# Kernel tuning notes

Measured on AMD Instinct MI355X. Metric: run time of the kernel, lower is better.

Reference implementation:

```python
import jax, jax.numpy as jnp
import numpy as np

N, E, T, D, V, G = 100000, 400000, 4, 300, 3000, 128
EPS = 1e-5


def _lin_init(k, fin, fout):
    s = 1.0 / np.sqrt(fin)
    kw, kb = jax.random.split(k)
    w = jax.random.uniform(kw, (fin, fout), jnp.float32, -s, s)
    b = jax.random.uniform(kb, (fout,), jnp.float32, -s, s)
    return w, b


def setup_inputs() -> dict:
    key = jax.random.key(0)
    ks = jax.random.split(key, 12)
    emb = jax.random.normal(ks[0], (V, D), jnp.float32) * 0.02
    emb = emb.at[0].set(0.0)  # padding_idx=0
    ew1, eb1 = _lin_init(ks[1], 3 * D, D)
    ew2, eb2 = _lin_init(ks[2], D, D)
    n1w1, n1b1 = _lin_init(ks[3], 2 * D, D)
    n1w2, n1b2 = _lin_init(ks[4], D, D)
    n2w1, n2b1 = _lin_init(ks[5], 2 * D, D)
    n2w2, n2b2 = _lin_init(ks[6], D, D)
    ln_w = jnp.ones((D,), jnp.float32)
    ln_b = jnp.zeros((D,), jnp.float32)
    x_tok = jax.random.randint(ks[7], (N, T), 0, V)
    edge_attr_tok = jax.random.randint(ks[8], (E, T), 0, V)
    edge_index = jax.random.randint(ks[9], (2, E), 0, N)
    added_sym_edge = jax.random.randint(ks[10], (E // 2,), 0, E)
    batch = jnp.sort(jax.random.randint(ks[11], (N,), 0, G))
    return dict(x_tok=x_tok, edge_attr_tok=edge_attr_tok, edge_index=edge_index,
                added_sym_edge=added_sym_edge, batch=batch, emb=emb,
                ew1=ew1, eb1=eb1, ew2=ew2, eb2=eb2,
                n1w1=n1w1, n1b1=n1b1, n1w2=n1w2, n1b2=n1b2,
                n2w1=n2w1, n2b1=n2b1, n2w2=n2w2, n2b2=n2b2,
                ln_w=ln_w, ln_b=ln_b)


def _mlp(h, w1, b1, w2, b2):
    return jnp.maximum(h @ w1 + b1, 0.0) @ w2 + b2


def reference(x_tok, edge_attr_tok, edge_index, added_sym_edge, batch, emb,
              ew1, eb1, ew2, eb2, n1w1, n1b1, n1w2, n1b2,
              n2w1, n2b1, n2w2, n2b2, ln_w, ln_b):
    # embedding-sum over token axis
    x = emb[x_tok].sum(axis=-2)                      # [N, D]
    sign = jnp.ones((E,), emb.dtype).at[added_sym_edge].set(-1.0)
    ea = (emb[edge_attr_tok] * sign[:, None, None]).sum(axis=-2)  # [E, D]

    row, col = edge_index[0], edge_index[1]
    # EdgeModel: cat([src, dest, edge_attr]) -> MLP
    e_in = jnp.concatenate([x[row], x[col], ea], axis=1)  # [E, 3D]
    edge_enc = _mlp(e_in, ew1, eb1, ew2, eb2)             # [E, D]

    # NodeModel: gather + MLP + scatter_mean + MLP
    m = _mlp(jnp.concatenate([x[row], edge_enc], axis=1), n1w1, n1b1, n1w2, n1b2)
    cnt = jax.ops.segment_sum(jnp.ones((E,), m.dtype), col, num_segments=N)
    agg = jax.ops.segment_sum(m, col, num_segments=N) / jnp.maximum(cnt, 1.0)[:, None]
    x_enc = _mlp(jnp.concatenate([x, agg], axis=1), n2w1, n2b1, n2w2, n2b2)  # [N, D]

    # GraphLayerNorm: normalize over all elements of each graph
    ncnt = jax.ops.segment_sum(jnp.ones((N,), x_enc.dtype), batch, num_segments=G)
    denom = jnp.maximum(ncnt * D, 1.0)
    mean = jax.ops.segment_sum(x_enc.sum(axis=-1), batch, num_segments=G) / denom
    xc = x_enc - mean[batch][:, None]
    var = jax.ops.segment_sum((xc * xc).sum(axis=-1), batch, num_segments=G) / denom
    x_out = xc / jnp.sqrt(var + EPS)[batch][:, None] * ln_w + ln_b
    return x_out, edge_enc
```

## Files before the change

kernel.cpp:

```cpp
#include <hip/hip_runtime.h>


constexpr int N_NODES = 100000;
constexpr int N_EDGES = 400000;
constexpr int TOKS    = 4;
constexpr int D       = 300;
constexpr int NG      = 128;
constexpr float EPSV  = 1e-5f;

typedef __attribute__((ext_vector_type(8))) short bh8;
typedef __attribute__((ext_vector_type(4))) float fx4;

constexpr size_t AGG_OFF  = 0;
constexpr size_t CNT_OFF  = AGG_OFF + (size_t)N_NODES * D;
constexpr size_t GSUM_OFF = CNT_OFF + N_NODES;
constexpr size_t GSQ_OFF  = GSUM_OFF + NG;
constexpr size_t GCNT_OFF = GSQ_OFF + NG;
constexpr size_t SIGN_OFF = GCNT_OFF + NG;
constexpr size_t X_OFF    = SIGN_OFF + N_EDGES;
constexpr size_t PACK_OFF = X_OFF + (size_t)N_NODES * D;
constexpr size_t ZERO_FLOATS = SIGN_OFF;

constexpr size_t P_SEC3 = 30ull * 20 * 64 * 8;
constexpr size_t P_SEC2 = 20ull * 20 * 64 * 8;
constexpr size_t P_SEC1 = 10ull * 20 * 64 * 8;

__device__ inline unsigned short f2bf(float f) {
    unsigned int u = __float_as_uint(f);
    return (unsigned short)((u + 0x7fffu + ((u >> 16) & 1u)) >> 16);
}
__device__ inline float bf2f(unsigned short s) {
    return __uint_as_float(((unsigned int)s) << 16);
}

__global__ void fill_sign_k(float* sign) {
    int i = blockIdx.x * blockDim.x + threadIdx.x;
    if (i < N_EDGES) sign[i] = 1.0f;
}

__global__ void scatter_sign_k(const int* __restrict__ ase, float* sign) {
    int i = blockIdx.x * blockDim.x + threadIdx.x;
    if (i < N_EDGES / 2) sign[ase[i]] = -1.0f;
}

__global__ void embsum_k(const int* __restrict__ tok, const float* __restrict__ emb,
                         const float* __restrict__ sign, float* out, int nrows) {
    int idx = blockIdx.x * blockDim.x + threadIdx.x;
    int total = nrows * D;
    if (idx >= total) return;
    int r = idx / D;
    int d = idx - r * D;
    const int* t = tok + r * TOKS;
    float s = emb[(size_t)t[0] * D + d] + emb[(size_t)t[1] * D + d]
            + emb[(size_t)t[2] * D + d] + emb[(size_t)t[3] * D + d];
    if (sign) s *= sign[r];
    out[idx] = s;
}

__global__ void count_col_k(const int* __restrict__ coli, float* cnt) {
    int i = blockIdx.x * blockDim.x + threadIdx.x;
    if (i < N_EDGES) atomicAdd(&cnt[coli[i]], 1.0f);
}

__global__ void pack_w_k(const float* __restrict__ W, unsigned short* __restrict__ out,
                         int secs) {
    int idx = blockIdx.x * blockDim.x + threadIdx.x;
    int total = secs * 12800;
    if (idx >= total) return;
    int lane = idx & 63;
    int nt = (idx >> 6) % 20;
    int kt = idx / 1280;
    int col = nt * 16 + (lane & 15);
    int kg = (lane >> 4) * 8;
#pragma unroll
    for (int j = 0; j < 8; ++j) {
        int p = kt * 32 + kg + j;
        int sec = p / 320;
        int kk = p - sec * 320;
        float w = 0.f;
        if (kk < 300 && col < 300) w = W[(size_t)(sec * 300 + kk) * 300 + col];
        out[(size_t)idx * 8 + j] = f2bf(w);
    }
}

template <int SECS, int MODE, bool SCATTER>
__global__ __launch_bounds__(256, 2) void mlp_mfma_k(
        const float* __restrict__ x, const float* aux,
        const int* __restrict__ rowi, const int* __restrict__ coli,
        const float* __restrict__ cnt,
        const unsigned short* __restrict__ W1p, const float* __restrict__ b1,
        const unsigned short* __restrict__ W2p, const float* __restrict__ b2,
        float* outp, int nrows)
{
    constexpr int NCHUNK = SECS * 5;
    __shared__ __align__(16) unsigned short Ahi[4096];
    __shared__ __align__(16) unsigned short Alo[4096];
    __shared__ __align__(16) unsigned short Hs[64 * 328];
    __shared__ int Ridx[64];
    __shared__ int Cidx[64];
    __shared__ float Icnt[64];

    const int tid  = threadIdx.x;
    const int wave = tid >> 6;
    const int lane = tid & 63;
    const int r0   = blockIdx.x * 64;

    if (tid < 64) {
        int e = r0 + tid; if (e >= nrows) e = nrows - 1;
        if constexpr (MODE == 0 || MODE == 1) { Ridx[tid] = rowi[e]; Cidx[tid] = coli[e]; }
        else { Icnt[tid] = 1.0f / fmaxf(cnt[e], 1.0f); }
    }
    for (int i = tid; i < 64 * 20; i += 256)
        Hs[(i / 20) * 328 + 300 + (i % 20)] = 0;
    __syncthreads();

    const int sm  = tid >> 2;
    const int sko = (tid & 3) << 4;
    const int skt   = sko >> 5;
    const int sg0   = (sko & 31) >> 3;
    const int smt   = sm >> 4;
    const int sbase = ((skt * 4 + smt) * 64 + (sm & 15) + sg0 * 16) * 8;
    int se = r0 + sm; if (se >= nrows) se = nrows - 1;

    fx4 acc[4][5];
#pragma unroll
    for (int a = 0; a < 4; ++a)
#pragma unroll
        for (int b = 0; b < 5; ++b) acc[a][b] = fx4{0.f, 0.f, 0.f, 0.f};

    for (int c = 0; c < NCHUNK; ++c) {
        {
            int sec = (c * 64) / 320;
            int kk0 = c * 64 - sec * 320 + sko;
            const float* base;
            if constexpr (MODE == 0) {
                base = (sec == 0) ? x + (size_t)Ridx[sm] * 300
                     : (sec == 1) ? x + (size_t)Cidx[sm] * 300
                                  : aux + (size_t)se * 300;
            } else if constexpr (MODE == 1) {
                base = (sec == 0) ? x + (size_t)Ridx[sm] * 300
                                  : aux + (size_t)se * 300;
            } else {
                base = (sec == 0) ? x + (size_t)se * 300 : aux + (size_t)se * 300;
            }
            float f[16];
            if (kk0 + 16 <= 300) {
                const float4* p = (const float4*)(base + kk0);
                float4 q0 = p[0], q1 = p[1], q2 = p[2], q3 = p[3];
                f[0]=q0.x; f[1]=q0.y; f[2]=q0.z; f[3]=q0.w;
                f[4]=q1.x; f[5]=q1.y; f[6]=q1.z; f[7]=q1.w;
                f[8]=q2.x; f[9]=q2.y; f[10]=q2.z; f[11]=q2.w;
                f[12]=q3.x; f[13]=q3.y; f[14]=q3.z; f[15]=q3.w;
            } else {
#pragma unroll
                for (int i = 0; i < 16; ++i) {
                    int kk = kk0 + i;
                    f[i] = (kk < 300) ? base[kk] : 0.f;
                }
            }
            if constexpr (MODE == 2) {
                float scale = (sec == 1) ? Icnt[sm] : 1.0f;
#pragma unroll
                for (int i = 0; i < 16; ++i) f[i] *= scale;
            }
            bh8 vh0, vl0, vh1, vl1;
#pragma unroll
            for (int i = 0; i < 8; ++i) {
                unsigned short h0 = f2bf(f[i]);
                vh0[i] = (short)h0;
                vl0[i] = (short)f2bf(f[i] - bf2f(h0));
                unsigned short h1 = f2bf(f[8 + i]);
                vh1[i] = (short)h1;
                vl1[i] = (short)f2bf(f[8 + i] - bf2f(h1));
            }
            *(bh8*)&Ahi[sbase]       = vh0;
            *(bh8*)&Ahi[sbase + 128] = vh1;
            *(bh8*)&Alo[sbase]       = vl0;
            *(bh8*)&Alo[sbase + 128] = vl1;
        }
        __syncthreads();
#pragma unroll
        for (int kt = 0; kt < 2; ++kt) {
            const int ktg = c * 2 + kt;
            bh8 bfr[5];
#pragma unroll
            for (int nt = 0; nt < 5; ++nt)
                bfr[nt] = *(const bh8*)(W1p + (((size_t)ktg * 20 + wave * 5 + nt) * 64 + lane) * 8);
#pragma unroll
            for (int mt = 0; mt < 4; ++mt) {
                bh8 ah = *(const bh8*)&Ahi[((kt * 4 + mt) * 64 + lane) * 8];
                bh8 al = *(const bh8*)&Alo[((kt * 4 + mt) * 64 + lane) * 8];
#pragma unroll
                for (int nt = 0; nt < 5; ++nt) {
                    acc[mt][nt] = __builtin_amdgcn_mfma_f32_16x16x32_bf16(ah, bfr[nt], acc[mt][nt], 0, 0, 0);
                    acc[mt][nt] = __builtin_amdgcn_mfma_f32_16x16x32_bf16(al, bfr[nt], acc[mt][nt], 0, 0, 0);
                }
            }
        }
        __syncthreads();
    }

    {
        const int rg = (lane >> 4) * 4;
#pragma unroll
        for (int nt = 0; nt < 5; ++nt) {
            int col = (wave * 5 + nt) * 16 + (lane & 15);
            if (col < 300) {
                float bb = b1[col];
#pragma unroll
                for (int mt = 0; mt < 4; ++mt)
#pragma unroll
                    for (int r = 0; r < 4; ++r) {
                        float v = fmaxf(acc[mt][nt][r] + bb, 0.f);
                        Hs[(mt * 16 + rg + r) * 328 + col] = f2bf(v);
                    }
            }
        }
    }
    __syncthreads();

    fx4 acc2[4][5];
#pragma unroll
    for (int a = 0; a < 4; ++a)
#pragma unroll
        for (int b = 0; b < 5; ++b) acc2[a][b] = fx4{0.f, 0.f, 0.f, 0.f};

    for (int kt = 0; kt < 10; ++kt) {
        bh8 bfr[5];
#pragma unroll
        for (int nt = 0; nt < 5; ++nt)
            bfr[nt] = *(const bh8*)(W2p + (((size_t)kt * 20 + wave * 5 + nt) * 64 + lane) * 8);
#pragma unroll
        for (int mt = 0; mt < 4; ++mt) {
            bh8 ah = *(const bh8*)&Hs[(mt * 16 + (lane & 15)) * 328 + kt * 32 + (lane >> 4) * 8];
#pragma unroll
            for (int nt = 0; nt < 5; ++nt)
                acc2[mt][nt] = __builtin_amdgcn_mfma_f32_16x16x32_bf16(ah, bfr[nt], acc2[mt][nt], 0, 0, 0);
        }
    }

    {
        const int rg = (lane >> 4) * 4;
#pragma unroll
        for (int nt = 0; nt < 5; ++nt) {
            int col = (wave * 5 + nt) * 16 + (lane & 15);
            if (col >= 300) continue;
            float bb = b2[col];
#pragma unroll
            for (int mt = 0; mt < 4; ++mt)
#pragma unroll
                for (int r = 0; r < 4; ++r) {
                    int m = mt * 16 + rg + r;
                    int e = r0 + m;
                    if (e >= nrows) continue;
                    float v = acc2[mt][nt][r] + bb;
                    if constexpr (SCATTER) atomicAdd(&outp[(size_t)Cidx[m] * 300 + col], v);
                    else                   outp[(size_t)e * 300 + col] = v;
                }
        }
    }
}

__global__ __launch_bounds__(256) void graph_stats_k(
        const float* __restrict__ xe, const int* __restrict__ batch,
        float* gsum, float* gsq, float* gcnt) {
    int n = blockIdx.x;
    int tid = threadIdx.x;
    float v = 0.f, v2 = 0.f;
    for (int d = tid; d < D; d += 256) {
        float t = xe[(size_t)n * D + d];
        v += t; v2 += t * t;
    }
    for (int off = 32; off > 0; off >>= 1) {
        v  += __shfl_down(v, off, 64);
        v2 += __shfl_down(v2, off, 64);
    }
    __shared__ float s1[4], s2[4];
    int w = tid >> 6, l = tid & 63;
    if (l == 0) { s1[w] = v; s2[w] = v2; }
    __syncthreads();
    if (tid == 0) {
        float a = s1[0] + s1[1] + s1[2] + s1[3];
        float b = s2[0] + s2[1] + s2[2] + s2[3];
        int g = batch[n];
        atomicAdd(&gsum[g], a);
        atomicAdd(&gsq[g], b);
        atomicAdd(&gcnt[g], 1.0f);
    }
}

__global__ void graph_norm_k(float* xe, const int* __restrict__ batch,
                             const float* __restrict__ gsum, const float* __restrict__ gsq,
                             const float* __restrict__ gcnt,
                             const float* __restrict__ lnw, const float* __restrict__ lnb) {
    int idx = blockIdx.x * blockDim.x + threadIdx.x;
    if (idx >= N_NODES * D) return;
    int n = idx / D;
    int d = idx - n * D;
    int g = batch[n];
    float denom = fmaxf(gcnt[g] * (float)D, 1.0f);
    float mean = gsum[g] / denom;
    float var  = gsq[g] / denom - mean * mean;
    float r = rsqrtf(var + EPSV);
    xe[idx] = (xe[idx] - mean) * r * lnw[d] + lnb[d];
}

extern "C" void kernel_launch(void* const* d_in, const int* in_sizes, int n_in,
                              void* d_out, int out_size, void* d_ws, size_t ws_size,
                              hipStream_t stream) {
    const int*   x_tok  = (const int*)d_in[0];
    const int*   ea_tok = (const int*)d_in[1];
    const int*   eidx   = (const int*)d_in[2];
    const int*   ase    = (const int*)d_in[3];
    const int*   batch  = (const int*)d_in[4];
    const float* emb    = (const float*)d_in[5];
    const float* ew1  = (const float*)d_in[6];
    const float* eb1  = (const float*)d_in[7];
    const float* ew2  = (const float*)d_in[8];
    const float* eb2  = (const float*)d_in[9];
    const float* n1w1 = (const float*)d_in[10];
    const float* n1b1 = (const float*)d_in[11];
    const float* n1w2 = (const float*)d_in[12];
    const float* n1b2 = (const float*)d_in[13];
    const float* n2w1 = (const float*)d_in[14];
    const float* n2b1 = (const float*)d_in[15];
    const float* n2w2 = (const float*)d_in[16];
    const float* n2b2 = (const float*)d_in[17];
    const float* lnw  = (const float*)d_in[18];
    const float* lnb  = (const float*)d_in[19];

    const int* rowi = eidx;
    const int* coli = eidx + N_EDGES;

    float* out  = (float*)d_out;
    float* xout = out;
    float* eenc = out + (size_t)N_NODES * D;

    float* ws   = (float*)d_ws;
    float* agg  = ws + AGG_OFF;
    float* cnt  = ws + CNT_OFF;
    float* gsum = ws + GSUM_OFF;
    float* gsq  = ws + GSQ_OFF;
    float* gcnt = ws + GCNT_OFF;
    float* sign = ws + SIGN_OFF;
    float* x    = ws + X_OFF;

    unsigned short* ew1p  = (unsigned short*)(ws + PACK_OFF);
    unsigned short* ew2p  = ew1p  + P_SEC3;
    unsigned short* n1w1p = ew2p  + P_SEC1;
    unsigned short* n1w2p = n1w1p + P_SEC2;
    unsigned short* n2w1p = n1w2p + P_SEC1;
    unsigned short* n2w2p = n2w1p + P_SEC2;

    pack_w_k<<<(3 * 12800 + 255) / 256, 256, 0, stream>>>(ew1,  ew1p,  3);
    pack_w_k<<<(1 * 12800 + 255) / 256, 256, 0, stream>>>(ew2,  ew2p,  1);
    pack_w_k<<<(2 * 12800 + 255) / 256, 256, 0, stream>>>(n1w1, n1w1p, 2);
    pack_w_k<<<(1 * 12800 + 255) / 256, 256, 0, stream>>>(n1w2, n1w2p, 1);
    pack_w_k<<<(2 * 12800 + 255) / 256, 256, 0, stream>>>(n2w1, n2w1p, 2);
    pack_w_k<<<(1 * 12800 + 255) / 256, 256, 0, stream>>>(n2w2, n2w2p, 1);

    hipMemsetAsync(ws, 0, ZERO_FLOATS * sizeof(float), stream);

    fill_sign_k<<<(N_EDGES + 255) / 256, 256, 0, stream>>>(sign);
    scatter_sign_k<<<(N_EDGES / 2 + 255) / 256, 256, 0, stream>>>(ase, sign);

    embsum_k<<<(N_NODES * D + 255) / 256, 256, 0, stream>>>(x_tok, emb, nullptr, x, N_NODES);
    embsum_k<<<(N_EDGES * D + 255) / 256, 256, 0, stream>>>(ea_tok, emb, sign, eenc, N_EDGES);

    mlp_mfma_k<3, 0, false><<<N_EDGES / 64, 256, 0, stream>>>(
        x, eenc, rowi, coli, nullptr, ew1p, eb1, ew2p, eb2, eenc, N_EDGES);

    count_col_k<<<(N_EDGES + 255) / 256, 256, 0, stream>>>(coli, cnt);

    mlp_mfma_k<2, 1, true><<<N_EDGES / 64, 256, 0, stream>>>(
        x, eenc, rowi, coli, nullptr, n1w1p, n1b1, n1w2p, n1b2, agg, N_EDGES);

    mlp_mfma_k<2, 2, false><<<(N_NODES + 63) / 64, 256, 0, stream>>>(
        x, agg, nullptr, nullptr, cnt, n2w1p, n2b1, n2w2p, n2b2, xout, N_NODES);

    graph_stats_k<<<N_NODES, 256, 0, stream>>>(xout, batch, gsum, gsq, gcnt);
    graph_norm_k<<<(N_NODES * D + 255) / 256, 256, 0, stream>>>(
        xout, batch, gsum, gsq, gcnt, lnw, lnb);
}
```

Measured before the change: 4.022 ms.

## Fuse edge embedding and graph stats into MLP kernels, double-buffer A tiles

```diff
diff --git a/kernel.cpp b/kernel.cpp
--- a/kernel.cpp
+++ b/kernel.cpp
@@ -3,7 +3,6 @@
 
 constexpr int N_NODES = 100000;
 constexpr int N_EDGES = 400000;
-constexpr int TOKS    = 4;
 constexpr int D       = 300;
 constexpr int NG      = 128;
 constexpr float EPSV  = 1e-5f;
@@ -29,9 +28,6 @@
     unsigned int u = __float_as_uint(f);
     return (unsigned short)((u + 0x7fffu + ((u >> 16) & 1u)) >> 16);
 }
-__device__ inline float bf2f(unsigned short s) {
-    return __uint_as_float(((unsigned int)s) << 16);
-}
 
 __global__ void fill_sign_k(float* sign) {
     int i = blockIdx.x * blockDim.x + threadIdx.x;
@@ -43,18 +39,22 @@
     if (i < N_EDGES / 2) sign[ase[i]] = -1.0f;
 }
 
-__global__ void embsum_k(const int* __restrict__ tok, const float* __restrict__ emb,
-                         const float* __restrict__ sign, float* out, int nrows) {
+__global__ void embsum4_k(const int* __restrict__ tok, const float* __restrict__ emb,
+                          float* out, int nrows) {
     int idx = blockIdx.x * blockDim.x + threadIdx.x;
-    int total = nrows * D;
+    int total = nrows * 75;
     if (idx >= total) return;
-    int r = idx / D;
-    int d = idx - r * D;
-    const int* t = tok + r * TOKS;
-    float s = emb[(size_t)t[0] * D + d] + emb[(size_t)t[1] * D + d]
-            + emb[(size_t)t[2] * D + d] + emb[(size_t)t[3] * D + d];
-    if (sign) s *= sign[r];
-    out[idx] = s;
+    int r = idx / 75;
+    int q = (idx - r * 75) * 4;
+    int4 t = *(const int4*)(tok + (size_t)r * 4);
+    float4 a = *(const float4*)(emb + (size_t)t.x * D + q);
+    float4 b = *(const float4*)(emb + (size_t)t.y * D + q);
+    float4 c = *(const float4*)(emb + (size_t)t.z * D + q);
+    float4 d = *(const float4*)(emb + (size_t)t.w * D + q);
+    float4 o;
+    o.x = a.x + b.x + c.x + d.x; o.y = a.y + b.y + c.y + d.y;
+    o.z = a.z + b.z + c.z + d.z; o.w = a.w + b.w + c.w + d.w;
+    *(float4*)(out + (size_t)r * D + q) = o;
 }
 
 __global__ void count_col_k(const int* __restrict__ coli, float* cnt) {
@@ -84,101 +84,139 @@
 }
 
 template <int SECS, int MODE, bool SCATTER>
-__global__ __launch_bounds__(256, 2) void mlp_mfma_k(
-        const float* __restrict__ x, const float* aux,
+__global__ __launch_bounds__(256, (MODE == 0) ? 2 : 3) void mlp_mfma_k(
+        const float* __restrict__ x, const float* __restrict__ aux,
         const int* __restrict__ rowi, const int* __restrict__ coli,
-        const float* __restrict__ cnt,
+        const float* __restrict__ cnt, const float* __restrict__ sign,
+        const int* __restrict__ eatok, const float* __restrict__ emb,
         const unsigned short* __restrict__ W1p, const float* __restrict__ b1,
         const unsigned short* __restrict__ W2p, const float* __restrict__ b2,
-        float* outp, int nrows)
+        float* outp, const int* __restrict__ batch,
+        float* gsum, float* gsq, float* gcnt, int nrows)
 {
     constexpr int NCHUNK = SECS * 5;
-    __shared__ __align__(16) unsigned short Ahi[4096];
-    __shared__ __align__(16) unsigned short Alo[4096];
-    __shared__ __align__(16) unsigned short Hs[64 * 328];
-    __shared__ int Ridx[64];
+    __shared__ __align__(16) unsigned short SM[20480];
     __shared__ int Cidx[64];
-    __shared__ float Icnt[64];
+    __shared__ float RS[64], RQ[64];
 
     const int tid  = threadIdx.x;
     const int wave = tid >> 6;
     const int lane = tid & 63;
     const int r0   = blockIdx.x * 64;
 
-    if (tid < 64) {
-        int e = r0 + tid; if (e >= nrows) e = nrows - 1;
-        if constexpr (MODE == 0 || MODE == 1) { Ridx[tid] = rowi[e]; Cidx[tid] = coli[e]; }
-        else { Icnt[tid] = 1.0f / fmaxf(cnt[e], 1.0f); }
-    }
-    for (int i = tid; i < 64 * 20; i += 256)
-        Hs[(i / 20) * 328 + 300 + (i % 20)] = 0;
-    __syncthreads();
-
     const int sm  = tid >> 2;
     const int sko = (tid & 3) << 4;
-    const int skt   = sko >> 5;
-    const int sg0   = (sko & 31) >> 3;
-    const int smt   = sm >> 4;
-    const int sbase = ((skt * 4 + smt) * 64 + (sm & 15) + sg0 * 16) * 8;
+    const int sbase = (((sko >> 5) * 4 + (sm >> 4)) * 64 + (sm & 15) + ((sko & 31) >> 3) * 16) * 8;
     int se = r0 + sm; if (se >= nrows) se = nrows - 1;
 
+    if (tid < 64) {
+        if constexpr (SCATTER) {
+            int e = r0 + tid; if (e >= nrows) e = nrows - 1;
+            Cidx[tid] = coli[e];
+        }
+        RS[tid] = 0.f; RQ[tid] = 0.f;
+    }
+
+    const float* sb0; const float* sb1;
+    const float *et0, *et1, *et2, *et3;
+    float sgn = 1.f, icnt = 1.f;
+    if constexpr (MODE == 0) {
+        sb0 = x + (size_t)rowi[se] * D;
+        sb1 = x + (size_t)coli[se] * D;
+        int4 tk = *(const int4*)(eatok + (size_t)se * 4);
+        et0 = emb + (size_t)tk.x * D; et1 = emb + (size_t)tk.y * D;
+        et2 = emb + (size_t)tk.z * D; et3 = emb + (size_t)tk.w * D;
+        sgn = sign[se];
+    } else if constexpr (MODE == 1) {
+        sb0 = x + (size_t)rowi[se] * D;
+        sb1 = aux + (size_t)se * D;
+    } else {
+        sb0 = x + (size_t)se * D;
+        sb1 = aux + (size_t)se * D;
+        icnt = 1.0f / fmaxf(cnt[se], 1.0f);
+    }
+
+    float4 G[(MODE == 0) ? 16 : 4];
+    float  f[16];
+
+    auto issuef = [&](int c) {
+        int s = c / 5;
+        int kk0 = (c - s * 5) * 64 + sko;
+        if constexpr (MODE == 0) {
+            if (s == 2) {
+#pragma unroll
+                for (int q = 0; q < 4; ++q) {
+                    int kk = kk0 + q * 4;
+                    bool ok = (kk + 4 <= 300);
+                    G[q]      = ok ? *(const float4*)(et0 + kk) : make_float4(0.f, 0.f, 0.f, 0.f);
+                    G[4 + q]  = ok ? *(const float4*)(et1 + kk) : make_float4(0.f, 0.f, 0.f, 0.f);
+                    G[8 + q]  = ok ? *(const float4*)(et2 + kk) : make_float4(0.f, 0.f, 0.f, 0.f);
+                    G[12 + q] = ok ? *(const float4*)(et3 + kk) : make_float4(0.f, 0.f, 0.f, 0.f);
+                }
+                return;
+            }
+        }
+        const float* b = (s == 0) ? sb0 : sb1;
+#pragma unroll
+        for (int q = 0; q < 4; ++q) {
+            int kk = kk0 + q * 4;
+            G[q] = (kk + 4 <= 300) ? *(const float4*)(b + kk) : make_float4(0.f, 0.f, 0.f, 0.f);
+        }
+    };
+
+    auto finishf = [&](int c) {
+        int s = c / 5;
+#pragma unroll
+        for (int q = 0; q < 4; ++q) {
+            float4 v = G[q];
+            if constexpr (MODE == 0) {
+                if (s == 2) {
+                    float4 t1 = G[4 + q], t2 = G[8 + q], t3 = G[12 + q];
+                    v.x = sgn * (v.x + t1.x + t2.x + t3.x);
+                    v.y = sgn * (v.y + t1.y + t2.y + t3.y);
+                    v.z = sgn * (v.z + t1.z + t2.z + t3.z);
+                    v.w = sgn * (v.w + t1.w + t2.w + t3.w);
+                }
+            }
+            if constexpr (MODE == 2) {
+                if (s == 1) { v.x *= icnt; v.y *= icnt; v.z *= icnt; v.w *= icnt; }
+            }
+            f[q * 4 + 0] = v.x; f[q * 4 + 1] = v.y; f[q * 4 + 2] = v.z; f[q * 4 + 3] = v.w;
+        }
+    };
+
+    auto convertf = [&](int buf) {
+        unsigned int uh[8], ul[8];
+#pragma unroll
+        for (int j = 0; j < 8; ++j) {
+            float a = f[2 * j], b = f[2 * j + 1];
+            unsigned int ua = __float_as_uint(a), ub = __float_as_uint(b);
+            uh[j] = __builtin_amdgcn_perm(ub, ua, 0x07060302u);
+            float la = a - __uint_as_float(ua & 0xffff0000u);
+            float lb = b - __uint_as_float(ub & 0xffff0000u);
+            ul[j] = __builtin_amdgcn_perm(__float_as_uint(lb), __float_as_uint(la), 0x07060302u);
+        }
+        int b0 = buf * 8192;
+        *(uint4*)&SM[b0 + sbase]              = make_uint4(uh[0], uh[1], uh[2], uh[3]);
+        *(uint4*)&SM[b0 + sbase + 128]        = make_uint4(uh[4], uh[5], uh[6], uh[7]);
+        *(uint4*)&SM[b0 + 4096 + sbase]       = make_uint4(ul[0], ul[1], ul[2], ul[3]);
+        *(uint4*)&SM[b0 + 4096 + sbase + 128] = make_uint4(ul[4], ul[5], ul[6], ul[7]);
+    };
+
     fx4 acc[4][5];
 #pragma unroll
     for (int a = 0; a < 4; ++a)
 #pragma unroll
         for (int b = 0; b < 5; ++b) acc[a][b] = fx4{0.f, 0.f, 0.f, 0.f};
 
+    issuef(0);
+    finishf(0);
+    convertf(0);
+    __syncthreads();
+
     for (int c = 0; c < NCHUNK; ++c) {
-        {
-            int sec = (c * 64) / 320;
-            int kk0 = c * 64 - sec * 320 + sko;
-            const float* base;
-            if constexpr (MODE == 0) {
-                base = (sec == 0) ? x + (size_t)Ridx[sm] * 300
-                     : (sec == 1) ? x + (size_t)Cidx[sm] * 300
-                                  : aux + (size_t)se * 300;
-            } else if constexpr (MODE == 1) {
-                base = (sec == 0) ? x + (size_t)Ridx[sm] * 300
-                                  : aux + (size_t)se * 300;
-            } else {
-                base = (sec == 0) ? x + (size_t)se * 300 : aux + (size_t)se * 300;
-            }
-            float f[16];
-            if (kk0 + 16 <= 300) {
-                const float4* p = (const float4*)(base + kk0);
-                float4 q0 = p[0], q1 = p[1], q2 = p[2], q3 = p[3];
-                f[0]=q0.x; f[1]=q0.y; f[2]=q0.z; f[3]=q0.w;
-                f[4]=q1.x; f[5]=q1.y; f[6]=q1.z; f[7]=q1.w;
-                f[8]=q2.x; f[9]=q2.y; f[10]=q2.z; f[11]=q2.w;
-                f[12]=q3.x; f[13]=q3.y; f[14]=q3.z; f[15]=q3.w;
-            } else {
-#pragma unroll
-                for (int i = 0; i < 16; ++i) {
-                    int kk = kk0 + i;
-                    f[i] = (kk < 300) ? base[kk] : 0.f;
-                }
-            }
-            if constexpr (MODE == 2) {
-                float scale = (sec == 1) ? Icnt[sm] : 1.0f;
-#pragma unroll
-                for (int i = 0; i < 16; ++i) f[i] *= scale;
-            }
-            bh8 vh0, vl0, vh1, vl1;
-#pragma unroll
-            for (int i = 0; i < 8; ++i) {
-                unsigned short h0 = f2bf(f[i]);
-                vh0[i] = (short)h0;
-                vl0[i] = (short)f2bf(f[i] - bf2f(h0));
-                unsigned short h1 = f2bf(f[8 + i]);
-                vh1[i] = (short)h1;
-                vl1[i] = (short)f2bf(f[8 + i] - bf2f(h1));
-            }
-            *(bh8*)&Ahi[sbase]       = vh0;
-            *(bh8*)&Ahi[sbase + 128] = vh1;
-            *(bh8*)&Alo[sbase]       = vl0;
-            *(bh8*)&Alo[sbase + 128] = vl1;
-        }
-        __syncthreads();
+        const int cur = c & 1;
+        if (c + 1 < NCHUNK) issuef(c + 1);
 #pragma unroll
         for (int kt = 0; kt < 2; ++kt) {
             const int ktg = c * 2 + kt;
@@ -188,8 +226,8 @@
                 bfr[nt] = *(const bh8*)(W1p + (((size_t)ktg * 20 + wave * 5 + nt) * 64 + lane) * 8);
 #pragma unroll
             for (int mt = 0; mt < 4; ++mt) {
-                bh8 ah = *(const bh8*)&Ahi[((kt * 4 + mt) * 64 + lane) * 8];
-                bh8 al = *(const bh8*)&Alo[((kt * 4 + mt) * 64 + lane) * 8];
+                bh8 ah = *(const bh8*)&SM[cur * 8192 + ((kt * 4 + mt) * 64 + lane) * 8];
+                bh8 al = *(const bh8*)&SM[cur * 8192 + 4096 + ((kt * 4 + mt) * 64 + lane) * 8];
 #pragma unroll
                 for (int nt = 0; nt < 5; ++nt) {
                     acc[mt][nt] = __builtin_amdgcn_mfma_f32_16x16x32_bf16(ah, bfr[nt], acc[mt][nt], 0, 0, 0);
@@ -197,33 +235,41 @@
                 }
             }
         }
+        if (c + 1 < NCHUNK) {
+            finishf(c + 1);
+            convertf(cur ^ 1);
+        }
         __syncthreads();
     }
 
+    const int rg = (lane >> 4) * 4;
+    for (int i = tid; i < 64 * 20; i += 256) {
+        int row = i / 20, h = 300 + (i % 20);
+        SM[((h >> 5) * 4 + ((h >> 3) & 3)) * 512 + row * 8 + (h & 7)] = 0;
+    }
     {
-        const int rg = (lane >> 4) * 4;
 #pragma unroll
         for (int nt = 0; nt < 5; ++nt) {
             int col = (wave * 5 + nt) * 16 + (lane & 15);
             if (col < 300) {
                 float bb = b1[col];
+                int hoff = ((col >> 5) * 4 + ((col >> 3) & 3)) * 512 + (col & 7);
 #pragma unroll
                 for (int mt = 0; mt < 4; ++mt)
 #pragma unroll
                     for (int r = 0; r < 4; ++r) {
                         float v = fmaxf(acc[mt][nt][r] + bb, 0.f);
-                        Hs[(mt * 16 + rg + r) * 328 + col] = f2bf(v);
+                        SM[hoff + (mt * 16 + rg + r) * 8] = f2bf(v);
                     }
             }
         }
     }
     __syncthreads();
 
-    fx4 acc2[4][5];
 #pragma unroll
     for (int a = 0; a < 4; ++a)
 #pragma unroll
-        for (int b = 0; b < 5; ++b) acc2[a][b] = fx4{0.f, 0.f, 0.f, 0.f};
+        for (int b = 0; b < 5; ++b) acc[a][b] = fx4{0.f, 0.f, 0.f, 0.f};
 
     for (int kt = 0; kt < 10; ++kt) {
         bh8 bfr[5];
@@ -232,77 +278,85 @@
             bfr[nt] = *(const bh8*)(W2p + (((size_t)kt * 20 + wave * 5 + nt) * 64 + lane) * 8);
 #pragma unroll
         for (int mt = 0; mt < 4; ++mt) {
-            bh8 ah = *(const bh8*)&Hs[(mt * 16 + (lane & 15)) * 328 + kt * 32 + (lane >> 4) * 8];
+            bh8 ah = *(const bh8*)&SM[((kt * 4 + (lane >> 4)) * 64 + mt * 16 + (lane & 15)) * 8];
 #pragma unroll
             for (int nt = 0; nt < 5; ++nt)
-                acc2[mt][nt] = __builtin_amdgcn_mfma_f32_16x16x32_bf16(ah, bfr[nt], acc2[mt][nt], 0, 0, 0);
-        }
-    }
-
-    {
-        const int rg = (lane >> 4) * 4;
-#pragma unroll
-        for (int nt = 0; nt < 5; ++nt) {
-            int col = (wave * 5 + nt) * 16 + (lane & 15);
-            if (col >= 300) continue;
-            float bb = b2[col];
-#pragma unroll
-            for (int mt = 0; mt < 4; ++mt)
-#pragma unroll
-                for (int r = 0; r < 4; ++r) {
-                    int m = mt * 16 + rg + r;
-                    int e = r0 + m;
-                    if (e >= nrows) continue;
-                    float v = acc2[mt][nt][r] + bb;
-                    if constexpr (SCATTER) atomicAdd(&outp[(size_t)Cidx[m] * 300 + col], v);
-                    else                   outp[(size_t)e * 300 + col] = v;
-                }
-        }
-    }
-}
-
-__global__ __launch_bounds__(256) void graph_stats_k(
-        const float* __restrict__ xe, const int* __restrict__ batch,
-        float* gsum, float* gsq, float* gcnt) {
-    int n = blockIdx.x;
-    int tid = threadIdx.x;
-    float v = 0.f, v2 = 0.f;
-    for (int d = tid; d < D; d += 256) {
-        float t = xe[(size_t)n * D + d];
-        v += t; v2 += t * t;
-    }
-    for (int off = 32; off > 0; off >>= 1) {
-        v  += __shfl_down(v, off, 64);
-        v2 += __shfl_down(v2, off, 64);
-    }
-    __shared__ float s1[4], s2[4];
-    int w = tid >> 6, l = tid & 63;
-    if (l == 0) { s1[w] = v; s2[w] = v2; }
-    __syncthreads();
-    if (tid == 0) {
-        float a = s1[0] + s1[1] + s1[2] + s1[3];
-        float b = s2[0] + s2[1] + s2[2] + s2[3];
-        int g = batch[n];
-        atomicAdd(&gsum[g], a);
-        atomicAdd(&gsq[g], b);
-        atomicAdd(&gcnt[g], 1.0f);
-    }
-}
-
-__global__ void graph_norm_k(float* xe, const int* __restrict__ batch,
-                             const float* __restrict__ gsum, const float* __restrict__ gsq,
-                             const float* __restrict__ gcnt,
-                             const float* __restrict__ lnw, const float* __restrict__ lnb) {
+                acc[mt][nt] = __builtin_amdgcn_mfma_f32_16x16x32_bf16(ah, bfr[nt], acc[mt][nt], 0, 0, 0);
+        }
+    }
+
+    float s1a[16], s2a[16];
+    if constexpr (MODE == 2) {
+#pragma unroll
+        for (int i = 0; i < 16; ++i) { s1a[i] = 0.f; s2a[i] = 0.f; }
+    }
+#pragma unroll
+    for (int nt = 0; nt < 5; ++nt) {
+        int col = (wave * 5 + nt) * 16 + (lane & 15);
+        if (col >= 300) continue;
+        float bb = b2[col];
+#pragma unroll
+        for (int mt = 0; mt < 4; ++mt)
+#pragma unroll
+            for (int r = 0; r < 4; ++r) {
+                int m = mt * 16 + rg + r;
+                int e = r0 + m;
+                if (e >= nrows) continue;
+                float v = acc[mt][nt][r] + bb;
+                if constexpr (SCATTER) atomicAdd(&outp[(size_t)Cidx[m] * D + col], v);
+                else                   outp[(size_t)e * D + col] = v;
+                if constexpr (MODE == 2) { s1a[mt * 4 + r] += v; s2a[mt * 4 + r] += v * v; }
+            }
+    }
+
+    if constexpr (MODE == 2) {
+#pragma unroll
+        for (int i = 0; i < 16; ++i) {
+            float s = s1a[i], q = s2a[i];
+            s += __shfl_xor(s, 1, 64); q += __shfl_xor(q, 1, 64);
+            s += __shfl_xor(s, 2, 64); q += __shfl_xor(q, 2, 64);
+            s += __shfl_xor(s, 4, 64); q += __shfl_xor(q, 4, 64);
+            s += __shfl_xor(s, 8, 64); q += __shfl_xor(q, 8, 64);
+            if ((lane & 15) == 0) {
+                int row = (i >> 2) * 16 + rg + (i & 3);
+                atomicAdd(&RS[row], s);
+                atomicAdd(&RQ[row], q);
+            }
+        }
+        __syncthreads();
+        if (tid < 64) {
+            int e = r0 + tid;
+            if (e < nrows) {
+                int g = batch[e];
+                atomicAdd(&gsum[g], RS[tid]);
+                atomicAdd(&gsq[g],  RQ[tid]);
+                atomicAdd(&gcnt[g], 1.0f);
+            }
+        }
+    }
+}
+
+__global__ void graph_norm4_k(float* xe, const int* __restrict__ batch,
+                              const float* __restrict__ gsum, const float* __restrict__ gsq,
+                              const float* __restrict__ gcnt,
+                              const float* __restrict__ lnw, const float* __restrict__ lnb) {
     int idx = blockIdx.x * blockDim.x + threadIdx.x;
-    if (idx >= N_NODES * D) return;
-    int n = idx / D;
-    int d = idx - n * D;
+    if (idx >= N_NODES * 75) return;
+    int n = idx / 75;
+    int d = (idx - n * 75) * 4;
     int g = batch[n];
     float denom = fmaxf(gcnt[g] * (float)D, 1.0f);
     float mean = gsum[g] / denom;
     float var  = gsq[g] / denom - mean * mean;
     float r = rsqrtf(var + EPSV);
-    xe[idx] = (xe[idx] - mean) * r * lnw[d] + lnb[d];
+    float4 v  = *(const float4*)(xe + (size_t)n * D + d);
+    float4 w  = *(const float4*)(lnw + d);
+    float4 bb = *(const float4*)(lnb + d);
+    v.x = (v.x - mean) * r * w.x + bb.x;
+    v.y = (v.y - mean) * r * w.y + bb.y;
+    v.z = (v.z - mean) * r * w.z + bb.z;
+    v.w = (v.w - mean) * r * w.w + bb.w;
+    *(float4*)(xe + (size_t)n * D + d) = v;
 }
 
 extern "C" void kernel_launch(void* const* d_in, const int* in_sizes, int n_in,
@@ -364,21 +418,22 @@
     fill_sign_k<<<(N_EDGES + 255) / 256, 256, 0, stream>>>(sign);
     scatter_sign_k<<<(N_EDGES / 2 + 255) / 256, 256, 0, stream>>>(ase, sign);
 
-    embsum_k<<<(N_NODES * D + 255) / 256, 256, 0, stream>>>(x_tok, emb, nullptr, x, N_NODES);
-    embsum_k<<<(N_EDGES * D + 255) / 256, 256, 0, stream>>>(ea_tok, emb, sign, eenc, N_EDGES);
+    embsum4_k<<<(N_NODES * 75 + 255) / 256, 256, 0, stream>>>(x_tok, emb, x, N_NODES);
 
     mlp_mfma_k<3, 0, false><<<N_EDGES / 64, 256, 0, stream>>>(
-        x, eenc, rowi, coli, nullptr, ew1p, eb1, ew2p, eb2, eenc, N_EDGES);
+        x, nullptr, rowi, coli, nullptr, sign, ea_tok, emb,
+        ew1p, eb1, ew2p, eb2, eenc, nullptr, nullptr, nullptr, nullptr, N_EDGES);
 
     count_col_k<<<(N_EDGES + 255) / 256, 256, 0, stream>>>(coli, cnt);
 
     mlp_mfma_k<2, 1, true><<<N_EDGES / 64, 256, 0, stream>>>(
-        x, eenc, rowi, coli, nullptr, n1w1p, n1b1, n1w2p, n1b2, agg, N_EDGES);
+        x, eenc, rowi, coli, nullptr, nullptr, nullptr, nullptr,
+        n1w1p, n1b1, n1w2p, n1b2, agg, nullptr, nullptr, nullptr, nullptr, N_EDGES);
 
     mlp_mfma_k<2, 2, false><<<(N_NODES + 63) / 64, 256, 0, stream>>>(
-        x, agg, nullptr, nullptr, cnt, n2w1p, n2b1, n2w2p, n2b2, xout, N_NODES);
-
-    graph_stats_k<<<N_NODES, 256, 0, stream>>>(xout, batch, gsum, gsq, gcnt);
-    graph_norm_k<<<(N_NODES * D + 255) / 256, 256, 0, stream>>>(
+        x, agg, nullptr, nullptr, cnt, nullptr, nullptr, nullptr,
+        n2w1p, n2b1, n2w2p, n2b2, xout, batch, gsum, gsq, gcnt, N_NODES);
+
+    graph_norm4_k<<<(N_NODES * 75 + 255) / 256, 256, 0, stream>>>(
         xout, batch, gsum, gsq, gcnt, lnw, lnb);
 }
```

Result: faster. 3.631 ms (-9.7%).
